# Kernel tuning notes

Hardware: AMD Instinct MI355X
Metric: run time of the kernel (lower is better)

## Reference

```python
import jax, jax.numpy as jnp
import numpy as np
from jax import lax


def _sobel_kernels(angle_deg, channel_n):
    dx = np.outer([1.0, 2.0, 1.0], [-1.0, 0.0, 1.0]) / 8.0
    dy = dx.T
    c = np.cos(angle_deg * np.pi / 180.0)
    s = np.sin(angle_deg * np.pi / 180.0)
    w1 = (c * dx - s * dy).astype(np.float32)
    w2 = (s * dx + c * dy).astype(np.float32)
    # depthwise kernels [C, 1, 3, 3] (OIHW with feature_group_count=C)
    k1 = jnp.tile(jnp.asarray(w1)[None, None], (channel_n, 1, 1, 1))
    k2 = jnp.tile(jnp.asarray(w2)[None, None], (channel_n, 1, 1, 1))
    return k1, k2


def _dwconv(x, k, groups):
    return lax.conv_general_dilated(
        x, k, window_strides=(1, 1), padding=[(1, 1), (1, 1)],
        feature_group_count=groups,
        dimension_numbers=('NCHW', 'OIHW', 'NCHW'))


def _maxpool3(x):
    # 3x3 max pool, stride 1, pad 1 over last two dims of NCHW
    return lax.reduce_window(x, -jnp.inf, lax.max,
                             (1, 1, 3, 3), (1, 1, 1, 1),
                             [(0, 0), (0, 0), (1, 1), (1, 1)])


def _alive(x_nchw):
    return _maxpool3(x_nchw[:, 3:4]) > 0.1


def _update(x, key, w0, b0, w1, wfr, k1, k2):
    # x: [B, H, W, C]  (torch does transpose(1,3) -> [B, C, W, H])
    xc = jnp.swapaxes(x, 1, 3)
    pre = _alive(xc)                               # [B,1,W,H] bool
    cn = xc.shape[1]
    y1 = _dwconv(xc, k1, cn)
    y2 = _dwconv(xc, k2, cn)
    dx = jnp.swapaxes(jnp.concatenate([xc, y1, y2], axis=1), 1, 3)  # [B,H,W,3C]
    fr = jax.nn.sigmoid(dx @ wfr.T) * jnp.swapaxes(pre, 1, 3)       # [B,H,W,1]
    log_fr = jnp.log(jnp.concatenate([fr, 1.0 - fr], axis=-1) + 1e-10)
    h = jax.nn.relu(dx @ w0.T + b0) @ w1.T                           # [B,H,W,C]
    # gumbel-softmax, tau=1, hard=True (straight-through)
    u = jax.random.uniform(key, log_fr.shape)
    g = -jnp.log(-jnp.log(u + 1e-20) + 1e-20)
    soft = jax.nn.softmax(log_fr + g, axis=-1)
    hard = jax.nn.one_hot(jnp.argmax(soft, axis=-1), 2, dtype=soft.dtype)
    update_grid = (hard + soft - lax.stop_gradient(soft))[..., 0:1]
    h = h * update_grid
    xc = xc + jnp.swapaxes(h, 1, 3)
    post = _alive(xc)
    xc = xc * (pre & post).astype(xc.dtype)
    return jnp.swapaxes(xc, 1, 3), fr[..., 0]


def setup_inputs() -> dict:
    key = jax.random.key(0)
    k = jax.random.split(key, 5)
    B, H, W, C, HID = 16, 128, 128, 16, 256
    return {
        'x': jax.random.uniform(k[0], (B, H, W, C), dtype=jnp.float32),
        'w0': jax.random.normal(k[1], (HID, 3 * C), dtype=jnp.float32) * 0.1,
        'b0': jax.random.normal(k[2], (HID,), dtype=jnp.float32) * 0.01,
        'w1': jax.random.normal(k[3], (C, HID), dtype=jnp.float32) * 0.1,
        'wfr': jax.random.normal(k[4], (1, 3 * C), dtype=jnp.float32) * 0.1,
        'steps': 4,
    }


def reference(x, w0, b0, w1, wfr, steps):
    angle = 0.0
    k1, k2 = _sobel_kernels(angle, x.shape[-1])
    keys = jax.random.split(jax.random.key(42), steps)

    def step(carry, key):
        xn, fr = _update(carry, key, w0, b0, w1, wfr, k1, k2)
        return xn, (xn, fr)

    _, (x_steps, fr_steps) = lax.scan(step, x, keys)
    return x_steps, fr_steps
```

## Files before the change

### kernel.cpp

```cpp
#include <hip/hip_runtime.h>
#include <cstdint>
#include <math.h>

#define HW2    16384
#define BHW    262144
#define XSLICE 4194304

__host__ __device__ static inline uint32_t rotl32(uint32_t v, int r) {
  return (v << r) | (v >> (32 - r));
}

__host__ __device__ static inline void tf2x32(uint32_t k0, uint32_t k1,
                                              uint32_t x0, uint32_t x1,
                                              uint32_t& o0, uint32_t& o1) {
  uint32_t ks2 = k0 ^ k1 ^ 0x1BD11BDAu;
  x0 += k0; x1 += k1;
#define TFR(r) { x0 += x1; x1 = rotl32(x1, (r)); x1 ^= x0; }
  TFR(13) TFR(15) TFR(26) TFR(6)   x0 += k1;  x1 += ks2 + 1u;
  TFR(17) TFR(29) TFR(16) TFR(24)  x0 += ks2; x1 += k0 + 2u;
  TFR(13) TFR(15) TFR(26) TFR(6)   x0 += k0;  x1 += k1 + 3u;
  TFR(17) TFR(29) TFR(16) TFR(24)  x0 += k1;  x1 += ks2 + 4u;
  TFR(13) TFR(15) TFR(26) TFR(6)   x0 += ks2; x1 += k0 + 5u;
#undef TFR
  o0 = x0; o1 = x1;
}

__device__ static inline float bits_to_unit(uint32_t bits) {
  return __uint_as_float((bits >> 9) | 0x3f800000u) - 1.0f;
}

__device__ static inline uint32_t rng_bits(uint32_t sk0, uint32_t sk1, uint32_t f) {
  uint32_t o0, o1;
  tf2x32(sk0, sk1, 0u, f, o0, o1);
  return o0 ^ o1;
}

__device__ static inline float sigmoidf_(float z) {
  if (z >= 0.f) { float e = expf(-z); return 1.f / (1.f + e); }
  float e = expf(z); return e / (1.f + e);
}

__device__ static inline void sobel_feat(const float* __restrict__ base,
                                         int hh, int ww, float* dxv, float& m3) {
#pragma unroll
  for (int c = 0; c < 48; ++c) dxv[c] = 0.f;
  m3 = -INFINITY;
#pragma unroll
  for (int dh = -1; dh <= 1; ++dh) {
    const int j = dh + 1;
    const int h2 = hh + dh;
    const bool hok = ((unsigned)h2 < 128u);
#pragma unroll
    for (int dw = -1; dw <= 1; ++dw) {
      const int i = dw + 1;
      const int w2 = ww + dw;
      float v[16];
      if (hok && ((unsigned)w2 < 128u)) {
        const float* s = base + (((h2 << 7) + w2) << 4);
#pragma unroll
        for (int c = 0; c < 16; c += 4) {
          float4 q = *(const float4*)(s + c);
          v[c] = q.x; v[c + 1] = q.y; v[c + 2] = q.z; v[c + 3] = q.w;
        }
        m3 = fmaxf(m3, v[3]);
      } else {
#pragma unroll
        for (int c = 0; c < 16; ++c) v[c] = 0.f;
      }
      const float smv[3] = {1.f, 2.f, 1.f};
      const float dfv[3] = {-1.f, 0.f, 1.f};
      const float c1 = smv[i] * dfv[j] * 0.125f;
      const float c2 = dfv[i] * smv[j] * 0.125f;
      if (dh == 0 && dw == 0) {
#pragma unroll
        for (int c = 0; c < 16; ++c) dxv[c] = v[c];
      }
      if (c1 != 0.f) {
#pragma unroll
        for (int c = 0; c < 16; ++c) dxv[16 + c] = fmaf(c1, v[c], dxv[16 + c]);
      }
      if (c2 != 0.f) {
#pragma unroll
        for (int c = 0; c < 16; ++c) dxv[32 + c] = fmaf(c2, v[c], dxv[32 + c]);
      }
    }
  }
}

__global__ __launch_bounds__(256, 2) void ca_step_a(
    const float* __restrict__ xin,
    const float* __restrict__ w0g,
    const float* __restrict__ b0g,
    const float* __restrict__ w1g,
    const float* __restrict__ wfrg,
    float* __restrict__ xmid,
    float* __restrict__ ch3,
    float* __restrict__ premask,
    float* __restrict__ frout,
    uint32_t sk0, uint32_t sk1) {
  __shared__ float sw[128 * 68];

  const int tid = threadIdx.x;
  const int p0  = blockIdx.x * 512 + tid;
  const int p1  = p0 + 256;
  const int b   = p0 >> 14;
  const int rem = p0 & 16383;
  const int hh0 = rem >> 7;
  const int ww0 = rem & 127;
  const int hh1 = hh0 + 2;

  const float* base = xin + ((size_t)b << 18);

  float dx0[48], dx1[48];
  float m30, m31;
  sobel_feat(base, hh0, ww0, dx0, m30);
  sobel_feat(base, hh1, ww0, dx1, m31);

  const bool pre0 = (m30 > 0.1f);
  const bool pre1 = (m31 > 0.1f);

  float z0 = 0.f, z1 = 0.f;
#pragma unroll
  for (int c = 0; c < 48; ++c) {
    z0 = fmaf(dx0[c], wfrg[c], z0);
    z1 = fmaf(dx1[c], wfrg[c], z1);
  }
  const float fr0 = pre0 ? sigmoidf_(z0) : 0.f;
  const float fr1 = pre1 ? sigmoidf_(z1) : 0.f;

  float upd0, upd1;
  {
    const float u0 = bits_to_unit(rng_bits(sk0, sk1, 2u * (uint32_t)p0));
    const float u1 = bits_to_unit(rng_bits(sk0, sk1, 2u * (uint32_t)p0 + 1u));
    const float d0 = logf(fr0 + 1e-10f) - logf(-logf(u0 + 1e-20f) + 1e-20f);
    const float d1 = logf(1.0f - fr0 + 1e-10f) - logf(-logf(u1 + 1e-20f) + 1e-20f);
    upd0 = (d0 >= d1) ? 1.f : 0.f;
  }
  {
    const float u0 = bits_to_unit(rng_bits(sk0, sk1, 2u * (uint32_t)p1));
    const float u1 = bits_to_unit(rng_bits(sk0, sk1, 2u * (uint32_t)p1 + 1u));
    const float d0 = logf(fr1 + 1e-10f) - logf(-logf(u0 + 1e-20f) + 1e-20f);
    const float d1 = logf(1.0f - fr1 + 1e-10f) - logf(-logf(u1 + 1e-20f) + 1e-20f);
    upd1 = (d0 >= d1) ? 1.f : 0.f;
  }

  float h0[16], h1[16];
#pragma unroll
  for (int c = 0; c < 16; ++c) { h0[c] = 0.f; h1[c] = 0.f; }

  for (int pass = 0; pass < 2; ++pass) {
    const int jb = pass << 7;
    if (pass) __syncthreads();
    {
      const float4* w04 = (const float4*)w0g;
      float4* sw4 = (float4*)sw;
      for (int i = tid; i < 1536; i += 256) {
        const int j = i / 12, q = i - j * 12;
        sw4[j * 17 + q] = w04[(jb + j) * 12 + q];
      }
      if (tid < 128) sw[tid * 68 + 48] = b0g[jb + tid];
      for (int i = tid; i < 2048; i += 256) {
        const int j = i & 127, c = i >> 7;
        sw[j * 68 + 52 + c] = w1g[c * 256 + jb + j];
      }
    }
    __syncthreads();
#pragma unroll 2
    for (int jj = 0; jj < 128; ++jj) {
      const float* row = sw + jj * 68;
      float a00 = 0.f, a01 = 0.f, a10 = 0.f, a11 = 0.f;
#pragma unroll
      for (int k = 0; k < 48; k += 8) {
        const float4 wa = *(const float4*)(row + k);
        const float4 wb = *(const float4*)(row + k + 4);
        a00 = fmaf(wa.x, dx0[k + 0], a00); a01 = fmaf(wa.y, dx0[k + 1], a01);
        a00 = fmaf(wa.z, dx0[k + 2], a00); a01 = fmaf(wa.w, dx0[k + 3], a01);
        a00 = fmaf(wb.x, dx0[k + 4], a00); a01 = fmaf(wb.y, dx0[k + 5], a01);
        a00 = fmaf(wb.z, dx0[k + 6], a00); a01 = fmaf(wb.w, dx0[k + 7], a01);
        a10 = fmaf(wa.x, dx1[k + 0], a10); a11 = fmaf(wa.y, dx1[k + 1], a11);
        a10 = fmaf(wa.z, dx1[k + 2], a10); a11 = fmaf(wa.w, dx1[k + 3], a11);
        a10 = fmaf(wb.x, dx1[k + 4], a10); a11 = fmaf(wb.y, dx1[k + 5], a11);
        a10 = fmaf(wb.z, dx1[k + 6], a10); a11 = fmaf(wb.w, dx1[k + 7], a11);
      }
      const float bb = row[48];
      const float r0 = fmaxf(bb + (a00 + a01), 0.f);
      const float r1 = fmaxf(bb + (a10 + a11), 0.f);
#pragma unroll
      for (int c = 0; c < 16; c += 4) {
        const float4 q = *(const float4*)(row + 52 + c);
        h0[c]     = fmaf(q.x, r0, h0[c]);     h1[c]     = fmaf(q.x, r1, h1[c]);
        h0[c + 1] = fmaf(q.y, r0, h0[c + 1]); h1[c + 1] = fmaf(q.y, r1, h1[c + 1]);
        h0[c + 2] = fmaf(q.z, r0, h0[c + 2]); h1[c + 2] = fmaf(q.z, r1, h1[c + 2]);
        h0[c + 3] = fmaf(q.w, r0, h0[c + 3]); h1[c + 3] = fmaf(q.w, r1, h1[c + 3]);
      }
    }
  }

  float* dst0 = xmid + ((size_t)p0 << 4);
  float* dst1 = xmid + ((size_t)p1 << 4);
#pragma unroll
  for (int c = 0; c < 16; c += 4) {
    float4 q0, q1;
    q0.x = fmaf(upd0, h0[c],     dx0[c]);     q1.x = fmaf(upd1, h1[c],     dx1[c]);
    q0.y = fmaf(upd0, h0[c + 1], dx0[c + 1]); q1.y = fmaf(upd1, h1[c + 1], dx1[c + 1]);
    q0.z = fmaf(upd0, h0[c + 2], dx0[c + 2]); q1.z = fmaf(upd1, h1[c + 2], dx1[c + 2]);
    q0.w = fmaf(upd0, h0[c + 3], dx0[c + 3]); q1.w = fmaf(upd1, h1[c + 3], dx1[c + 3]);
    *(float4*)(dst0 + c) = q0;
    *(float4*)(dst1 + c) = q1;
  }
  ch3[p0]     = fmaf(upd0, h0[3], dx0[3]);
  ch3[p1]     = fmaf(upd1, h1[3], dx1[3]);
  premask[p0] = pre0 ? 1.f : 0.f;
  premask[p1] = pre1 ? 1.f : 0.f;
  frout[p0]   = fr0;
  frout[p1]   = fr1;
}

__global__ __launch_bounds__(256) void ca_step_b(
    float* __restrict__ xs, const float* __restrict__ ch3,
    const float* __restrict__ premask) {
  const int p   = blockIdx.x * 256 + threadIdx.x;
  const int b   = p >> 14;
  const int rem = p & 16383;
  const int hh  = rem >> 7;
  const int ww  = rem & 127;
  const float* cb = ch3 + (b << 14);
  float m = -INFINITY;
#pragma unroll
  for (int dh = -1; dh <= 1; ++dh) {
    const int h2 = hh + dh;
    if ((unsigned)h2 >= 128u) continue;
#pragma unroll
    for (int dw = -1; dw <= 1; ++dw) {
      const int w2 = ww + dw;
      if ((unsigned)w2 >= 128u) continue;
      m = fmaxf(m, cb[(h2 << 7) + w2]);
    }
  }
  const bool alive = (premask[p] != 0.f) && (m > 0.1f);
  if (!alive) {
    float4 z; z.x = 0.f; z.y = 0.f; z.z = 0.f; z.w = 0.f;
    float* dst = xs + ((size_t)p << 4);
    *(float4*)(dst)      = z;
    *(float4*)(dst + 4)  = z;
    *(float4*)(dst + 8)  = z;
    *(float4*)(dst + 12) = z;
  }
}

extern "C" void kernel_launch(void* const* d_in, const int* in_sizes, int n_in,
                              void* d_out, int out_size, void* d_ws, size_t ws_size,
                              hipStream_t stream) {
  const float* x0  = (const float*)d_in[0];
  const float* w0  = (const float*)d_in[1];
  const float* b0  = (const float*)d_in[2];
  const float* w1  = (const float*)d_in[3];
  const float* wfr = (const float*)d_in[4];
  const int steps = 4;

  float* xsteps  = (float*)d_out;
  float* frsteps = xsteps + (size_t)steps * XSLICE;

  float* ch3 = (float*)d_ws;
  float* pre = ch3 + BHW;

  uint32_t sk[4][2];
  for (int s = 0; s < steps; ++s)
    tf2x32(0u, 42u, 0u, (uint32_t)s, sk[s][0], sk[s][1]);

  for (int s = 0; s < steps; ++s) {
    const float* xin = (s == 0) ? x0 : (xsteps + (size_t)(s - 1) * XSLICE);
    float* xmid = xsteps + (size_t)s * XSLICE;
    ca_step_a<<<512, 256, 0, stream>>>(xin, w0, b0, w1, wfr, xmid, ch3, pre,
                                       frsteps + (size_t)s * BHW, sk[s][0], sk[s][1]);
    ca_step_b<<<1024, 256, 0, stream>>>(xmid, ch3, pre);
  }
}
```

Before: 505.1 us.

## Split weight operands between LDS and wave-uniform scalar global loads

Only the first half of each w0 row goes into shared memory now. The second half of w0, the bias and a pre-transposed w1 are read straight from global memory through uniform pointers, with an asm trick so the compiler treats them as scalar loads. The aim is to cut LDS traffic and footprint in the hidden-layer loop by moving operand reads onto the scalar memory path. This adds a small transpose kernel launch and depends on scalar cache hit rates and on the compiler actually emitting s_load instructions.

```diff
diff --git a/kernel.cpp b/kernel.cpp
--- a/kernel.cpp
+++ b/kernel.cpp
@@ -91,16 +91,19 @@
     const float* __restrict__ xin,
     const float* __restrict__ w0g,
     const float* __restrict__ b0g,
-    const float* __restrict__ w1g,
+    const float* __restrict__ w1tg,
     const float* __restrict__ wfrg,
     float* __restrict__ xmid,
     float* __restrict__ ch3,
     float* __restrict__ premask,
     float* __restrict__ frout,
     uint32_t sk0, uint32_t sk1) {
-  __shared__ float sw[128 * 68];
+  __shared__ float sw0[128 * 24];
 
   const int tid = threadIdx.x;
+  int lz = 0;
+  asm volatile("" : "+v"(lz));
+
   const int p0  = blockIdx.x * 512 + tid;
   const int p1  = p0 + 256;
   const int b   = p0 >> 14;
@@ -148,31 +151,32 @@
 #pragma unroll
   for (int c = 0; c < 16; ++c) { h0[c] = 0.f; h1[c] = 0.f; }
 
+  const float4* __restrict__ w0u = (const float4*)w0g + lz;
+  const float*  __restrict__ b0v = b0g + lz;
+  const float4* __restrict__ w1v = (const float4*)w1tg + lz;
+
   for (int pass = 0; pass < 2; ++pass) {
     const int jb = pass << 7;
     if (pass) __syncthreads();
     {
       const float4* w04 = (const float4*)w0g;
-      float4* sw4 = (float4*)sw;
-      for (int i = tid; i < 1536; i += 256) {
-        const int j = i / 12, q = i - j * 12;
-        sw4[j * 17 + q] = w04[(jb + j) * 12 + q];
-      }
-      if (tid < 128) sw[tid * 68 + 48] = b0g[jb + tid];
-      for (int i = tid; i < 2048; i += 256) {
-        const int j = i & 127, c = i >> 7;
-        sw[j * 68 + 52 + c] = w1g[c * 256 + jb + j];
+      float4* sw4 = (float4*)sw0;
+      for (int i = tid; i < 768; i += 256) {
+        const int j = i / 6, q = i - j * 6;
+        sw4[j * 6 + q] = w04[(jb + j) * 12 + q];
       }
     }
     __syncthreads();
 #pragma unroll 2
     for (int jj = 0; jj < 128; ++jj) {
-      const float* row = sw + jj * 68;
+      const float*  rowl = sw0 + jj * 24;
+      const float4* rowu = w0u + (size_t)(jb + jj) * 12 + 6;
       float a00 = 0.f, a01 = 0.f, a10 = 0.f, a11 = 0.f;
 #pragma unroll
-      for (int k = 0; k < 48; k += 8) {
-        const float4 wa = *(const float4*)(row + k);
-        const float4 wb = *(const float4*)(row + k + 4);
+      for (int ks = 0; ks < 3; ++ks) {
+        const int k = ks * 8;
+        const float4 wa = *(const float4*)(rowl + k);
+        const float4 wb = *(const float4*)(rowl + k + 4);
         a00 = fmaf(wa.x, dx0[k + 0], a00); a01 = fmaf(wa.y, dx0[k + 1], a01);
         a00 = fmaf(wa.z, dx0[k + 2], a00); a01 = fmaf(wa.w, dx0[k + 3], a01);
         a00 = fmaf(wb.x, dx0[k + 4], a00); a01 = fmaf(wb.y, dx0[k + 5], a01);
@@ -182,12 +186,28 @@
         a10 = fmaf(wb.x, dx1[k + 4], a10); a11 = fmaf(wb.y, dx1[k + 5], a11);
         a10 = fmaf(wb.z, dx1[k + 6], a10); a11 = fmaf(wb.w, dx1[k + 7], a11);
       }
-      const float bb = row[48];
+#pragma unroll
+      for (int ks = 0; ks < 3; ++ks) {
+        const int k = 24 + ks * 8;
+        const float4 wa = rowu[ks * 2];
+        const float4 wb = rowu[ks * 2 + 1];
+        a00 = fmaf(wa.x, dx0[k + 0], a00); a01 = fmaf(wa.y, dx0[k + 1], a01);
+        a00 = fmaf(wa.z, dx0[k + 2], a00); a01 = fmaf(wa.w, dx0[k + 3], a01);
+        a00 = fmaf(wb.x, dx0[k + 4], a00); a01 = fmaf(wb.y, dx0[k + 5], a01);
+        a00 = fmaf(wb.z, dx0[k + 6], a00); a01 = fmaf(wb.w, dx0[k + 7], a01);
+        a10 = fmaf(wa.x, dx1[k + 0], a10); a11 = fmaf(wa.y, dx1[k + 1], a11);
+        a10 = fmaf(wa.z, dx1[k + 2], a10); a11 = fmaf(wa.w, dx1[k + 3], a11);
+        a10 = fmaf(wb.x, dx1[k + 4], a10); a11 = fmaf(wb.y, dx1[k + 5], a11);
+        a10 = fmaf(wb.z, dx1[k + 6], a10); a11 = fmaf(wb.w, dx1[k + 7], a11);
+      }
+      const float bb = b0v[jb + jj];
       const float r0 = fmaxf(bb + (a00 + a01), 0.f);
       const float r1 = fmaxf(bb + (a10 + a11), 0.f);
-#pragma unroll
-      for (int c = 0; c < 16; c += 4) {
-        const float4 q = *(const float4*)(row + 52 + c);
+      const float4* w1r = w1v + ((size_t)(jb + jj) << 2);
+#pragma unroll
+      for (int c4 = 0; c4 < 4; ++c4) {
+        const float4 q = w1r[c4];
+        const int c = c4 << 2;
         h0[c]     = fmaf(q.x, r0, h0[c]);     h1[c]     = fmaf(q.x, r1, h1[c]);
         h0[c + 1] = fmaf(q.y, r0, h0[c + 1]); h1[c + 1] = fmaf(q.y, r1, h1[c + 1]);
         h0[c + 2] = fmaf(q.z, r0, h0[c + 2]); h1[c + 2] = fmaf(q.z, r1, h1[c + 2]);
@@ -248,6 +268,15 @@
   }
 }
 
+__global__ void w1_transpose(const float* __restrict__ w1, float* __restrict__ w1t) {
+  const int i = blockIdx.x * 256 + threadIdx.x;
+  if (i < 4096) {
+    const int c = i >> 8;
+    const int jj = i & 255;
+    w1t[jj * 16 + c] = w1[i];
+  }
+}
+
 extern "C" void kernel_launch(void* const* d_in, const int* in_sizes, int n_in,
                               void* d_out, int out_size, void* d_ws, size_t ws_size,
                               hipStream_t stream) {
@@ -261,17 +290,19 @@
   float* xsteps  = (float*)d_out;
   float* frsteps = xsteps + (size_t)steps * XSLICE;
 
-  float* ch3 = (float*)d_ws;
+  float* w1t = (float*)d_ws;
+  float* ch3 = w1t + 4096;
   float* pre = ch3 + BHW;
 
   uint32_t sk[4][2];
   for (int s = 0; s < steps; ++s)
     tf2x32(0u, 42u, 0u, (uint32_t)s, sk[s][0], sk[s][1]);
 
+  w1_transpose<<<16, 256, 0, stream>>>(w1, w1t);
   for (int s = 0; s < steps; ++s) {
     const float* xin = (s == 0) ? x0 : (xsteps + (size_t)(s - 1) * XSLICE);
     float* xmid = xsteps + (size_t)s * XSLICE;
-    ca_step_a<<<512, 256, 0, stream>>>(xin, w0, b0, w1, wfr, xmid, ch3, pre,
+    ca_step_a<<<512, 256, 0, stream>>>(xin, w0, b0, w1t, wfr, xmid, ch3, pre,
                                        frsteps + (size_t)s * BHW, sk[s][0], sk[s][1]);
     ca_step_b<<<1024, 256, 0, stream>>>(xmid, ch3, pre);
   }
```

Result: slower. 818.7 us (+62.1%).

## Read w0 rows as uniform scalar loads and pack w1/bias into a shared table

Applied to the files above, without the earlier changes.

The w0 rows are no longer staged in shared memory. Each thread loads them straight from global memory with uniform addresses into double-buffered register arrays, so the compiler can use scalar (SGPR) loads that are prefetched one neuron ahead. A new one-time pack kernel transposes w1 and appends b0 into a compact 256x20 table, which each block copies into LDS once. This removes the two-pass shared staging, its barriers and most LDS reads in the hidden-layer loop. The risks are extra register pressure from two 48-float weight buffers and reliance on the compiler actually emitting scalar loads.

```diff
diff --git a/kernel.cpp b/kernel.cpp
--- a/kernel.cpp
+++ b/kernel.cpp
@@ -90,17 +90,24 @@
 __global__ __launch_bounds__(256, 2) void ca_step_a(
     const float* __restrict__ xin,
     const float* __restrict__ w0g,
-    const float* __restrict__ b0g,
-    const float* __restrict__ w1g,
+    const float* __restrict__ w1pg,
     const float* __restrict__ wfrg,
     float* __restrict__ xmid,
     float* __restrict__ ch3,
     float* __restrict__ premask,
     float* __restrict__ frout,
     uint32_t sk0, uint32_t sk1) {
-  __shared__ float sw[128 * 68];
+  __shared__ float sw1[256 * 20];
 
   const int tid = threadIdx.x;
+  {
+    const float4* src = (const float4*)w1pg;
+    float4* dst = (float4*)sw1;
+#pragma unroll
+    for (int i = 0; i < 5; ++i) dst[tid + 256 * i] = src[tid + 256 * i];
+  }
+  __syncthreads();
+
   const int p0  = blockIdx.x * 512 + tid;
   const int p1  = p0 + 256;
   const int b   = p0 >> 14;
@@ -148,53 +155,47 @@
 #pragma unroll
   for (int c = 0; c < 16; ++c) { h0[c] = 0.f; h1[c] = 0.f; }
 
-  for (int pass = 0; pass < 2; ++pass) {
-    const int jb = pass << 7;
-    if (pass) __syncthreads();
+#define NEURON(J, W)                                                         \
+  {                                                                          \
+    const float* rw = sw1 + (J) * 20;                                        \
+    float a00 = 0.f, a01 = 0.f, a10 = 0.f, a11 = 0.f;                        \
+    _Pragma("unroll")                                                        \
+    for (int k = 0; k < 48; k += 2) {                                        \
+      a00 = fmaf(W[k], dx0[k], a00);     a01 = fmaf(W[k + 1], dx0[k + 1], a01); \
+      a10 = fmaf(W[k], dx1[k], a10);     a11 = fmaf(W[k + 1], dx1[k + 1], a11); \
+    }                                                                        \
+    const float bb = rw[16];                                                 \
+    const float r0 = fmaxf(bb + (a00 + a01), 0.f);                           \
+    const float r1 = fmaxf(bb + (a10 + a11), 0.f);                           \
+    _Pragma("unroll")                                                        \
+    for (int c = 0; c < 16; c += 4) {                                        \
+      const float4 q = *(const float4*)(rw + c);                             \
+      h0[c]     = fmaf(q.x, r0, h0[c]);     h1[c]     = fmaf(q.x, r1, h1[c]);     \
+      h0[c + 1] = fmaf(q.y, r0, h0[c + 1]); h1[c + 1] = fmaf(q.y, r1, h1[c + 1]); \
+      h0[c + 2] = fmaf(q.z, r0, h0[c + 2]); h1[c + 2] = fmaf(q.z, r1, h1[c + 2]); \
+      h0[c + 3] = fmaf(q.w, r0, h0[c + 3]); h1[c + 3] = fmaf(q.w, r1, h1[c + 3]); \
+    }                                                                        \
+  }
+
+  float wA[48], wB[48];
+#pragma unroll
+  for (int q = 0; q < 48; ++q) wA[q] = w0g[q];
+
+  for (int jj = 0; jj < 256; jj += 2) {
     {
-      const float4* w04 = (const float4*)w0g;
-      float4* sw4 = (float4*)sw;
-      for (int i = tid; i < 1536; i += 256) {
-        const int j = i / 12, q = i - j * 12;
-        sw4[j * 17 + q] = w04[(jb + j) * 12 + q];
-      }
-      if (tid < 128) sw[tid * 68 + 48] = b0g[jb + tid];
-      for (int i = tid; i < 2048; i += 256) {
-        const int j = i & 127, c = i >> 7;
-        sw[j * 68 + 52 + c] = w1g[c * 256 + jb + j];
-      }
-    }
-    __syncthreads();
-#pragma unroll 2
-    for (int jj = 0; jj < 128; ++jj) {
-      const float* row = sw + jj * 68;
-      float a00 = 0.f, a01 = 0.f, a10 = 0.f, a11 = 0.f;
-#pragma unroll
-      for (int k = 0; k < 48; k += 8) {
-        const float4 wa = *(const float4*)(row + k);
-        const float4 wb = *(const float4*)(row + k + 4);
-        a00 = fmaf(wa.x, dx0[k + 0], a00); a01 = fmaf(wa.y, dx0[k + 1], a01);
-        a00 = fmaf(wa.z, dx0[k + 2], a00); a01 = fmaf(wa.w, dx0[k + 3], a01);
-        a00 = fmaf(wb.x, dx0[k + 4], a00); a01 = fmaf(wb.y, dx0[k + 5], a01);
-        a00 = fmaf(wb.z, dx0[k + 6], a00); a01 = fmaf(wb.w, dx0[k + 7], a01);
-        a10 = fmaf(wa.x, dx1[k + 0], a10); a11 = fmaf(wa.y, dx1[k + 1], a11);
-        a10 = fmaf(wa.z, dx1[k + 2], a10); a11 = fmaf(wa.w, dx1[k + 3], a11);
-        a10 = fmaf(wb.x, dx1[k + 4], a10); a11 = fmaf(wb.y, dx1[k + 5], a11);
-        a10 = fmaf(wb.z, dx1[k + 6], a10); a11 = fmaf(wb.w, dx1[k + 7], a11);
-      }
-      const float bb = row[48];
-      const float r0 = fmaxf(bb + (a00 + a01), 0.f);
-      const float r1 = fmaxf(bb + (a10 + a11), 0.f);
-#pragma unroll
-      for (int c = 0; c < 16; c += 4) {
-        const float4 q = *(const float4*)(row + 52 + c);
-        h0[c]     = fmaf(q.x, r0, h0[c]);     h1[c]     = fmaf(q.x, r1, h1[c]);
-        h0[c + 1] = fmaf(q.y, r0, h0[c + 1]); h1[c + 1] = fmaf(q.y, r1, h1[c + 1]);
-        h0[c + 2] = fmaf(q.z, r0, h0[c + 2]); h1[c + 2] = fmaf(q.z, r1, h1[c + 2]);
-        h0[c + 3] = fmaf(q.w, r0, h0[c + 3]); h1[c + 3] = fmaf(q.w, r1, h1[c + 3]);
-      }
-    }
-  }
+      const float* __restrict__ nr = w0g + (jj + 1) * 48;
+#pragma unroll
+      for (int q = 0; q < 48; ++q) wB[q] = nr[q];
+    }
+    NEURON(jj, wA)
+    {
+      const float* __restrict__ nr = w0g + ((jj + 2) & 255) * 48;
+#pragma unroll
+      for (int q = 0; q < 48; ++q) wA[q] = nr[q];
+    }
+    NEURON(jj + 1, wB)
+  }
+#undef NEURON
 
   float* dst0 = xmid + ((size_t)p0 << 4);
   float* dst1 = xmid + ((size_t)p1 << 4);
@@ -248,6 +249,19 @@
   }
 }
 
+__global__ void pack_w1(const float* __restrict__ w1, const float* __restrict__ b0,
+                        float* __restrict__ w1p) {
+  const int j = blockIdx.x * 256 + threadIdx.x;
+  if (j < 256) {
+#pragma unroll
+    for (int c = 0; c < 16; ++c) w1p[j * 20 + c] = w1[c * 256 + j];
+    w1p[j * 20 + 16] = b0[j];
+    w1p[j * 20 + 17] = 0.f;
+    w1p[j * 20 + 18] = 0.f;
+    w1p[j * 20 + 19] = 0.f;
+  }
+}
+
 extern "C" void kernel_launch(void* const* d_in, const int* in_sizes, int n_in,
                               void* d_out, int out_size, void* d_ws, size_t ws_size,
                               hipStream_t stream) {
@@ -261,17 +275,19 @@
   float* xsteps  = (float*)d_out;
   float* frsteps = xsteps + (size_t)steps * XSLICE;
 
-  float* ch3 = (float*)d_ws;
+  float* w1p = (float*)d_ws;
+  float* ch3 = w1p + 5120;
   float* pre = ch3 + BHW;
 
   uint32_t sk[4][2];
   for (int s = 0; s < steps; ++s)
     tf2x32(0u, 42u, 0u, (uint32_t)s, sk[s][0], sk[s][1]);
 
+  pack_w1<<<1, 256, 0, stream>>>(w1, b0, w1p);
   for (int s = 0; s < steps; ++s) {
     const float* xin = (s == 0) ? x0 : (xsteps + (size_t)(s - 1) * XSLICE);
     float* xmid = xsteps + (size_t)s * XSLICE;
-    ca_step_a<<<512, 256, 0, stream>>>(xin, w0, b0, w1, wfr, xmid, ch3, pre,
+    ca_step_a<<<512, 256, 0, stream>>>(xin, w0, w1p, wfr, xmid, ch3, pre,
                                        frsteps + (size_t)s * BHW, sk[s][0], sk[s][1]);
     ca_step_b<<<1024, 256, 0, stream>>>(xmid, ch3, pre);
   }
```

After: 573.2 us. 13.5% more time.

## Process four pixels per thread and pre-pack w1/b0 for coalesced smem loads

Applied to the files above, without the earlier changes.

Each thread now computes four pixels instead of two, so every shared-memory weight row read is reused across four feature vectors, and the grid halves to 256 blocks. A small pre-kernel packs w1 transposed together with b0 into a padded row layout, letting the shared-memory fill become one float4 loop. The cost is far higher register pressure (launch bounds drop to one block per CU, four 48-float feature arrays), and only 256 blocks may underfill the GPU's CUs.

```diff
diff --git a/kernel.cpp b/kernel.cpp
--- a/kernel.cpp
+++ b/kernel.cpp
@@ -87,11 +87,10 @@
   }
 }
 
-__global__ __launch_bounds__(256, 2) void ca_step_a(
+__global__ __launch_bounds__(256, 1) void ca_step_a(
     const float* __restrict__ xin,
     const float* __restrict__ w0g,
-    const float* __restrict__ b0g,
-    const float* __restrict__ w1g,
+    const float* __restrict__ w1pg,
     const float* __restrict__ wfrg,
     float* __restrict__ xmid,
     float* __restrict__ ch3,
@@ -101,67 +100,70 @@
   __shared__ float sw[128 * 68];
 
   const int tid = threadIdx.x;
-  const int p0  = blockIdx.x * 512 + tid;
-  const int p1  = p0 + 256;
+  const int p0  = blockIdx.x * 1024 + tid;
   const int b   = p0 >> 14;
   const int rem = p0 & 16383;
   const int hh0 = rem >> 7;
   const int ww0 = rem & 127;
-  const int hh1 = hh0 + 2;
 
   const float* base = xin + ((size_t)b << 18);
 
-  float dx0[48], dx1[48];
-  float m30, m31;
-  sobel_feat(base, hh0, ww0, dx0, m30);
-  sobel_feat(base, hh1, ww0, dx1, m31);
+  float dx0[48], dx1[48], dx2[48], dx3[48];
+  float m30, m31, m32, m33;
+  sobel_feat(base, hh0,     ww0, dx0, m30);
+  sobel_feat(base, hh0 + 2, ww0, dx1, m31);
+  sobel_feat(base, hh0 + 4, ww0, dx2, m32);
+  sobel_feat(base, hh0 + 6, ww0, dx3, m33);
 
   const bool pre0 = (m30 > 0.1f);
   const bool pre1 = (m31 > 0.1f);
-
-  float z0 = 0.f, z1 = 0.f;
+  const bool pre2 = (m32 > 0.1f);
+  const bool pre3 = (m33 > 0.1f);
+
+  float z0 = 0.f, z1 = 0.f, z2 = 0.f, z3 = 0.f;
 #pragma unroll
   for (int c = 0; c < 48; ++c) {
-    z0 = fmaf(dx0[c], wfrg[c], z0);
-    z1 = fmaf(dx1[c], wfrg[c], z1);
+    const float wf = wfrg[c];
+    z0 = fmaf(dx0[c], wf, z0);
+    z1 = fmaf(dx1[c], wf, z1);
+    z2 = fmaf(dx2[c], wf, z2);
+    z3 = fmaf(dx3[c], wf, z3);
   }
   const float fr0 = pre0 ? sigmoidf_(z0) : 0.f;
   const float fr1 = pre1 ? sigmoidf_(z1) : 0.f;
-
-  float upd0, upd1;
-  {
-    const float u0 = bits_to_unit(rng_bits(sk0, sk1, 2u * (uint32_t)p0));
-    const float u1 = bits_to_unit(rng_bits(sk0, sk1, 2u * (uint32_t)p0 + 1u));
-    const float d0 = logf(fr0 + 1e-10f) - logf(-logf(u0 + 1e-20f) + 1e-20f);
-    const float d1 = logf(1.0f - fr0 + 1e-10f) - logf(-logf(u1 + 1e-20f) + 1e-20f);
-    upd0 = (d0 >= d1) ? 1.f : 0.f;
-  }
-  {
-    const float u0 = bits_to_unit(rng_bits(sk0, sk1, 2u * (uint32_t)p1));
-    const float u1 = bits_to_unit(rng_bits(sk0, sk1, 2u * (uint32_t)p1 + 1u));
-    const float d0 = logf(fr1 + 1e-10f) - logf(-logf(u0 + 1e-20f) + 1e-20f);
-    const float d1 = logf(1.0f - fr1 + 1e-10f) - logf(-logf(u1 + 1e-20f) + 1e-20f);
-    upd1 = (d0 >= d1) ? 1.f : 0.f;
-  }
-
-  float h0[16], h1[16];
-#pragma unroll
-  for (int c = 0; c < 16; ++c) { h0[c] = 0.f; h1[c] = 0.f; }
+  const float fr2 = pre2 ? sigmoidf_(z2) : 0.f;
+  const float fr3 = pre3 ? sigmoidf_(z3) : 0.f;
+
+#define GATE(FR, P, OUT)                                                       \
+  {                                                                            \
+    const float u0 = bits_to_unit(rng_bits(sk0, sk1, 2u * (uint32_t)(P)));     \
+    const float u1 = bits_to_unit(rng_bits(sk0, sk1, 2u * (uint32_t)(P) + 1u));\
+    const float d0 = logf((FR) + 1e-10f) - logf(-logf(u0 + 1e-20f) + 1e-20f);  \
+    const float d1 = logf(1.0f - (FR) + 1e-10f) - logf(-logf(u1 + 1e-20f) + 1e-20f); \
+    OUT = (d0 >= d1) ? 1.f : 0.f;                                              \
+  }
+  float upd0, upd1, upd2, upd3;
+  GATE(fr0, p0,        upd0)
+  GATE(fr1, p0 + 256,  upd1)
+  GATE(fr2, p0 + 512,  upd2)
+  GATE(fr3, p0 + 768,  upd3)
+#undef GATE
+
+  float h0[16], h1[16], h2[16], h3[16];
+#pragma unroll
+  for (int c = 0; c < 16; ++c) { h0[c] = 0.f; h1[c] = 0.f; h2[c] = 0.f; h3[c] = 0.f; }
 
   for (int pass = 0; pass < 2; ++pass) {
     const int jb = pass << 7;
     if (pass) __syncthreads();
     {
-      const float4* w04 = (const float4*)w0g;
+      const float4* w04  = (const float4*)w0g;
+      const float4* w1p4 = (const float4*)w1pg;
       float4* sw4 = (float4*)sw;
-      for (int i = tid; i < 1536; i += 256) {
-        const int j = i / 12, q = i - j * 12;
-        sw4[j * 17 + q] = w04[(jb + j) * 12 + q];
-      }
-      if (tid < 128) sw[tid * 68 + 48] = b0g[jb + tid];
-      for (int i = tid; i < 2048; i += 256) {
-        const int j = i & 127, c = i >> 7;
-        sw[j * 68 + 52 + c] = w1g[c * 256 + jb + j];
+      for (int i = tid; i < 2176; i += 256) {
+        const int j = i / 17, q = i - j * 17;
+        sw4[i] = (q < 12) ? w04[(jb + j) * 12 + q]
+                          : w1p4[(jb + j) * 5 + (q - 12)];
       }
     }
     __syncthreads();
@@ -169,8 +171,10 @@
     for (int jj = 0; jj < 128; ++jj) {
       const float* row = sw + jj * 68;
       float a00 = 0.f, a01 = 0.f, a10 = 0.f, a11 = 0.f;
-#pragma unroll
-      for (int k = 0; k < 48; k += 8) {
+      float a20 = 0.f, a21 = 0.f, a30 = 0.f, a31 = 0.f;
+#pragma unroll
+      for (int ks = 0; ks < 6; ++ks) {
+        const int k = ks * 8;
         const float4 wa = *(const float4*)(row + k);
         const float4 wb = *(const float4*)(row + k + 4);
         a00 = fmaf(wa.x, dx0[k + 0], a00); a01 = fmaf(wa.y, dx0[k + 1], a01);
@@ -181,39 +185,57 @@
         a10 = fmaf(wa.z, dx1[k + 2], a10); a11 = fmaf(wa.w, dx1[k + 3], a11);
         a10 = fmaf(wb.x, dx1[k + 4], a10); a11 = fmaf(wb.y, dx1[k + 5], a11);
         a10 = fmaf(wb.z, dx1[k + 6], a10); a11 = fmaf(wb.w, dx1[k + 7], a11);
-      }
-      const float bb = row[48];
+        a20 = fmaf(wa.x, dx2[k + 0], a20); a21 = fmaf(wa.y, dx2[k + 1], a21);
+        a20 = fmaf(wa.z, dx2[k + 2], a20); a21 = fmaf(wa.w, dx2[k + 3], a21);
+        a20 = fmaf(wb.x, dx2[k + 4], a20); a21 = fmaf(wb.y, dx2[k + 5], a21);
+        a20 = fmaf(wb.z, dx2[k + 6], a20); a21 = fmaf(wb.w, dx2[k + 7], a21);
+        a30 = fmaf(wa.x, dx3[k + 0], a30); a31 = fmaf(wa.y, dx3[k + 1], a31);
+        a30 = fmaf(wa.z, dx3[k + 2], a30); a31 = fmaf(wa.w, dx3[k + 3], a31);
+        a30 = fmaf(wb.x, dx3[k + 4], a30); a31 = fmaf(wb.y, dx3[k + 5], a31);
+        a30 = fmaf(wb.z, dx3[k + 6], a30); a31 = fmaf(wb.w, dx3[k + 7], a31);
+      }
+      const float bb = row[64];
       const float r0 = fmaxf(bb + (a00 + a01), 0.f);
       const float r1 = fmaxf(bb + (a10 + a11), 0.f);
-#pragma unroll
-      for (int c = 0; c < 16; c += 4) {
-        const float4 q = *(const float4*)(row + 52 + c);
+      const float r2 = fmaxf(bb + (a20 + a21), 0.f);
+      const float r3 = fmaxf(bb + (a30 + a31), 0.f);
+#pragma unroll
+      for (int c4 = 0; c4 < 4; ++c4) {
+        const float4 q = *(const float4*)(row + 48 + (c4 << 2));
+        const int c = c4 << 2;
         h0[c]     = fmaf(q.x, r0, h0[c]);     h1[c]     = fmaf(q.x, r1, h1[c]);
         h0[c + 1] = fmaf(q.y, r0, h0[c + 1]); h1[c + 1] = fmaf(q.y, r1, h1[c + 1]);
         h0[c + 2] = fmaf(q.z, r0, h0[c + 2]); h1[c + 2] = fmaf(q.z, r1, h1[c + 2]);
         h0[c + 3] = fmaf(q.w, r0, h0[c + 3]); h1[c + 3] = fmaf(q.w, r1, h1[c + 3]);
+        h2[c]     = fmaf(q.x, r2, h2[c]);     h3[c]     = fmaf(q.x, r3, h3[c]);
+        h2[c + 1] = fmaf(q.y, r2, h2[c + 1]); h3[c + 1] = fmaf(q.y, r3, h3[c + 1]);
+        h2[c + 2] = fmaf(q.z, r2, h2[c + 2]); h3[c + 2] = fmaf(q.z, r3, h3[c + 2]);
+        h2[c + 3] = fmaf(q.w, r2, h2[c + 3]); h3[c + 3] = fmaf(q.w, r3, h3[c + 3]);
       }
     }
   }
 
-  float* dst0 = xmid + ((size_t)p0 << 4);
-  float* dst1 = xmid + ((size_t)p1 << 4);
-#pragma unroll
-  for (int c = 0; c < 16; c += 4) {
-    float4 q0, q1;
-    q0.x = fmaf(upd0, h0[c],     dx0[c]);     q1.x = fmaf(upd1, h1[c],     dx1[c]);
-    q0.y = fmaf(upd0, h0[c + 1], dx0[c + 1]); q1.y = fmaf(upd1, h1[c + 1], dx1[c + 1]);
-    q0.z = fmaf(upd0, h0[c + 2], dx0[c + 2]); q1.z = fmaf(upd1, h1[c + 2], dx1[c + 2]);
-    q0.w = fmaf(upd0, h0[c + 3], dx0[c + 3]); q1.w = fmaf(upd1, h1[c + 3], dx1[c + 3]);
-    *(float4*)(dst0 + c) = q0;
-    *(float4*)(dst1 + c) = q1;
-  }
-  ch3[p0]     = fmaf(upd0, h0[3], dx0[3]);
-  ch3[p1]     = fmaf(upd1, h1[3], dx1[3]);
-  premask[p0] = pre0 ? 1.f : 0.f;
-  premask[p1] = pre1 ? 1.f : 0.f;
-  frout[p0]   = fr0;
-  frout[p1]   = fr1;
+#define EPILOG(PX, DX, H, UPD, PRE, FR)                                        \
+  {                                                                            \
+    float* dst = xmid + ((size_t)(PX) << 4);                                   \
+    _Pragma("unroll")                                                          \
+    for (int c = 0; c < 16; c += 4) {                                          \
+      float4 q;                                                                \
+      q.x = fmaf(UPD, H[c],     DX[c]);                                        \
+      q.y = fmaf(UPD, H[c + 1], DX[c + 1]);                                    \
+      q.z = fmaf(UPD, H[c + 2], DX[c + 2]);                                    \
+      q.w = fmaf(UPD, H[c + 3], DX[c + 3]);                                    \
+      *(float4*)(dst + c) = q;                                                 \
+    }                                                                          \
+    ch3[PX]     = fmaf(UPD, H[3], DX[3]);                                      \
+    premask[PX] = (PRE) ? 1.f : 0.f;                                           \
+    frout[PX]   = FR;                                                          \
+  }
+  EPILOG(p0,       dx0, h0, upd0, pre0, fr0)
+  EPILOG(p0 + 256, dx1, h1, upd1, pre1, fr1)
+  EPILOG(p0 + 512, dx2, h2, upd2, pre2, fr2)
+  EPILOG(p0 + 768, dx3, h3, upd3, pre3, fr3)
+#undef EPILOG
 }
 
 __global__ __launch_bounds__(256) void ca_step_b(
@@ -248,6 +270,19 @@
   }
 }
 
+__global__ void pack_w1(const float* __restrict__ w1, const float* __restrict__ b0,
+                        float* __restrict__ w1p) {
+  const int j = blockIdx.x * 256 + threadIdx.x;
+  if (j < 256) {
+#pragma unroll
+    for (int c = 0; c < 16; ++c) w1p[j * 20 + c] = w1[c * 256 + j];
+    w1p[j * 20 + 16] = b0[j];
+    w1p[j * 20 + 17] = 0.f;
+    w1p[j * 20 + 18] = 0.f;
+    w1p[j * 20 + 19] = 0.f;
+  }
+}
+
 extern "C" void kernel_launch(void* const* d_in, const int* in_sizes, int n_in,
                               void* d_out, int out_size, void* d_ws, size_t ws_size,
                               hipStream_t stream) {
@@ -261,17 +296,19 @@
   float* xsteps  = (float*)d_out;
   float* frsteps = xsteps + (size_t)steps * XSLICE;
 
-  float* ch3 = (float*)d_ws;
+  float* w1p = (float*)d_ws;
+  float* ch3 = w1p + 5120;
   float* pre = ch3 + BHW;
 
   uint32_t sk[4][2];
   for (int s = 0; s < steps; ++s)
     tf2x32(0u, 42u, 0u, (uint32_t)s, sk[s][0], sk[s][1]);
 
+  pack_w1<<<1, 256, 0, stream>>>(w1, b0, w1p);
   for (int s = 0; s < steps; ++s) {
     const float* xin = (s == 0) ? x0 : (xsteps + (size_t)(s - 1) * XSLICE);
     float* xmid = xsteps + (size_t)s * XSLICE;
-    ca_step_a<<<512, 256, 0, stream>>>(xin, w0, b0, w1, wfr, xmid, ch3, pre,
+    ca_step_a<<<256, 256, 0, stream>>>(xin, w0, w1p, wfr, xmid, ch3, pre,
                                        frsteps + (size_t)s * BHW, sk[s][0], sk[s][1]);
     ca_step_b<<<1024, 256, 0, stream>>>(xmid, ch3, pre);
   }
```

Result: slower. 1.103 ms (+118.4%).
